# Performance work log

Measured on AMD Instinct MI355X. Metric: run time of the kernel, lower is better.

Reference implementation:

```python
import jax, jax.numpy as jnp
import numpy as np

HEAD_SIZE = 64
N_EMB = 384
B, S = 512, 256

def setup_inputs() -> dict:
    key = jax.random.key(0)
    k1, k2, k3, k4 = jax.random.split(key, 4)
    x = jax.random.normal(k1, (B, S, N_EMB), dtype=jnp.float32)
    scale = 1.0 / np.sqrt(N_EMB)
    Wq = jax.random.normal(k2, (N_EMB, HEAD_SIZE), dtype=jnp.float32) * scale
    Wk = jax.random.normal(k3, (N_EMB, HEAD_SIZE), dtype=jnp.float32) * scale
    Wv = jax.random.normal(k4, (N_EMB, HEAD_SIZE), dtype=jnp.float32) * scale
    return {"x": x, "Wq": Wq, "Wk": Wk, "Wv": Wv}

def reference(x, Wq, Wk, Wv):
    # Projections (Linear, no bias): [B,S,E] @ [E,H] -> [B,S,H]
    q = jnp.einsum('bse,eh->bsh', x, Wq)
    k = jnp.einsum('bse,eh->bsh', x, Wk)
    v = jnp.einsum('bse,eh->bsh', x, Wv)
    # Scores: [B,S,S], scaled by 1/sqrt(head_size)
    scores = jnp.einsum('bqh,bkh->bqk', q, k) / jnp.sqrt(jnp.asarray(HEAD_SIZE, x.dtype))
    seq_len = x.shape[1]
    causal = jnp.tril(jnp.ones((seq_len, seq_len), dtype=bool))
    scores = jnp.where(causal[None, :, :], scores, jnp.asarray(-jnp.inf, scores.dtype))
    attn = jax.nn.softmax(scores, axis=-1)
    # dropout_ratio=0 -> identity
    out = jnp.einsum('bqk,bkh->bqh', attn, v)
    return out
```

## Files before the change

kernel.cpp:

```cpp
#include <hip/hip_runtime.h>
#include <hip/hip_bf16.h>


#define NB   512
#define SS   256
#define EE   384
#define HH   64

#define PR16  16
#define LROW  392
#define XLSZ  (PR16 * LROW)

typedef short bf16x8 __attribute__((ext_vector_type(8)));
typedef float f32x4  __attribute__((ext_vector_type(4)));

__device__ __forceinline__ short f2bf(float f) {
  union { float f; unsigned u; } x; x.f = f;
  unsigned r = x.u + 0x7fffu + ((x.u >> 16) & 1u);
  return (short)(r >> 16);
}

__global__ __launch_bounds__(256) void prep_w_kernel(
    const float* __restrict__ Wq, const float* __restrict__ Wk,
    const float* __restrict__ Wv, short* __restrict__ wfrag) {
  int t = blockIdx.x * 256 + threadIdx.x;
  if (t >= 12 * 12 * 64) return;
  int ks  = t / (12 * 64);
  int rem = t % (12 * 64);
  int nf  = rem / 64;
  int l   = rem % 64;
  int l15 = l & 15, lhi = l >> 4;
  int ncat = nf * 16 + l15;
  const float* W = (ncat < 64) ? Wq : (ncat < 128 ? Wk : Wv);
  int n = ncat & 63;
  short* dst = wfrag + (size_t)t * 8;
#pragma unroll
  for (int j = 0; j < 8; ++j) {
    int kk = ks * 32 + lhi * 8 + j;
    dst[j] = f2bf(W[kk * 64 + n]);
  }
}

__global__ __launch_bounds__(512, 2) void fused_kernel(
    const float* __restrict__ x, const short* __restrict__ wfrag,
    float* __restrict__ out) {
  __shared__ short Ql[SS * HH];
  __shared__ short Kl[SS * HH];
  __shared__ short Vt[HH * SS];
  __shared__ short scratch[4 * XLSZ];

  int b    = blockIdx.x;
  int tid  = threadIdx.x;
  int lane = tid & 63, wv = tid >> 6;
  int l15  = lane & 15, lhi = lane >> 4;
  int g    = wv >> 2;
  int wg   = wv & 3;
  int tg   = tid & 255;
  const float* xg = x + (size_t)b * SS * EE + (size_t)g * 128 * EE;

  bf16x8 af[12][3];
#pragma unroll
  for (int ks = 0; ks < 12; ++ks)
#pragma unroll
    for (int h = 0; h < 3; ++h)
      af[ks][h] = *(const bf16x8*)(wfrag + ((size_t)(ks * 12 + wg * 3 + h) * 64 + lane) * 8);

  f32x4 st[6];

  auto loadch = [&](int ch) {
    const float* p0 = xg + (size_t)ch * (PR16 * EE);
#pragma unroll
    for (int i = 0; i < 3; ++i) {
      const f32x4* p = (const f32x4*)(p0 + (size_t)(tg + 256 * i) * 8);
      st[2 * i]     = p[0];
      st[2 * i + 1] = p[1];
    }
  };
  auto writech = [&](short* xl) {
#pragma unroll
    for (int i = 0; i < 3; ++i) {
      int c = tg + 256 * i;
      int row = c / 48, cg = c % 48;
      union { bf16x8 vv; __hip_bfloat162 h2[4]; } u;
      u.h2[0] = __float22bfloat162_rn(make_float2(st[2*i][0],   st[2*i][1]));
      u.h2[1] = __float22bfloat162_rn(make_float2(st[2*i][2],   st[2*i][3]));
      u.h2[2] = __float22bfloat162_rn(make_float2(st[2*i+1][0], st[2*i+1][1]));
      u.h2[3] = __float22bfloat162_rn(make_float2(st[2*i+1][2], st[2*i+1][3]));
      *(bf16x8*)(xl + row * LROW + cg * 8) = u.vv;
    }
  };

  loadch(0);
  writech(scratch + (g * 2) * XLSZ);

  for (int ch = 0; ch < 8; ++ch) {
    __syncthreads();
    if (ch < 7) loadch(ch + 1);
    const short* xl = scratch + (g * 2 + (ch & 1)) * XLSZ;

    f32x4 acc[3];
#pragma unroll
    for (int h = 0; h < 3; ++h) acc[h] = (f32x4){0.f, 0.f, 0.f, 0.f};

#pragma unroll
    for (int ks = 0; ks < 12; ++ks) {
      bf16x8 bx = *(const bf16x8*)(xl + l15 * LROW + ks * 32 + lhi * 8);
#pragma unroll
      for (int h = 0; h < 3; ++h)
        acc[h] = __builtin_amdgcn_mfma_f32_16x16x32_bf16(af[ks][h], bx, acc[h], 0, 0, 0);
    }

    int ncb = wg * 48 + lhi * 4;
    int row = g * 128 + ch * PR16 + l15;
#pragma unroll
    for (int ht = 0; ht < 3; ++ht) {
      int ncat = ncb + ht * 16;
      if (ncat < 128) {
        short* dst = (ncat < 64) ? Ql : Kl;
        int col = ncat & 63;
        union { short4 s4; __hip_bfloat162 h2[2]; } o;
        o.h2[0] = __float22bfloat162_rn(make_float2(acc[ht][0], acc[ht][1]));
        o.h2[1] = __float22bfloat162_rn(make_float2(acc[ht][2], acc[ht][3]));
        *(short4*)(dst + row * 64 + (col ^ ((row & 7) << 3))) = o.s4;
      } else {
#pragma unroll
        for (int j = 0; j < 4; ++j) {
          int h = ncat - 128 + j;
          Vt[h * 256 + (row ^ ((h & 7) << 3))] = f2bf(acc[ht][j]);
        }
      }
    }
    if (ch < 7) writech(scratch + (g * 2 + ((ch + 1) & 1)) * XLSZ);
  }
  __syncthreads();

  bf16x8 qa[2][2];
#pragma unroll
  for (int u = 0; u < 2; ++u) {
    int rt  = (u == 0) ? wv : (15 - wv);
    int row = rt * 16 + l15;
#pragma unroll
    for (int kf = 0; kf < 2; ++kf)
      qa[u][kf] = *(const bf16x8*)(Ql + row * 64 + ((kf * 32 + lhi * 8) ^ ((row & 7) << 3)));
  }
  __syncthreads();

  short* P = (wv < 6) ? (scratch + wv * (16 * 256)) : (Ql + (wv - 6) * (16 * 256));
  size_t obase = (size_t)b * SS * HH;

#pragma unroll
  for (int u = 0; u < 2; ++u) {
    int rt    = (u == 0) ? wv : (15 - wv);
    int qrow0 = rt * 16;
    int twp   = (rt + 2) & ~1;

    f32x4 s[16];
#pragma unroll
    for (int t = 0; t < 16; ++t) {
      if (t >= twp) continue;
      int kc = t * 16 + l15;
      bf16x8 kb0 = *(const bf16x8*)(Kl + kc * 64 + ((lhi * 8)      ^ ((kc & 7) << 3)));
      bf16x8 kb1 = *(const bf16x8*)(Kl + kc * 64 + ((32 + lhi * 8) ^ ((kc & 7) << 3)));
      f32x4 a = (f32x4){0.f, 0.f, 0.f, 0.f};
      a = __builtin_amdgcn_mfma_f32_16x16x32_bf16(qa[u][0], kb0, a, 0, 0, 0);
      a = __builtin_amdgcn_mfma_f32_16x16x32_bf16(qa[u][1], kb1, a, 0, 0, 0);
      s[t] = a;
    }

#pragma unroll
    for (int t = 0; t < 16; ++t) {
      if (t >= twp) continue;
      int col = t * 16 + l15;
#pragma unroll
      for (int r = 0; r < 4; ++r) {
        int qg = qrow0 + lhi * 4 + r;
        float val = s[t][r] * 0.125f;
        s[t][r] = (col > qg) ? -INFINITY : val;
      }
    }
    float mx[4], sm[4], inv[4];
#pragma unroll
    for (int r = 0; r < 4; ++r) mx[r] = -INFINITY;
#pragma unroll
    for (int t = 0; t < 16; ++t) {
      if (t >= twp) continue;
#pragma unroll
      for (int r = 0; r < 4; ++r) mx[r] = fmaxf(mx[r], s[t][r]);
    }
#pragma unroll
    for (int r = 0; r < 4; ++r) {
      mx[r] = fmaxf(mx[r], __shfl_xor(mx[r], 1));
      mx[r] = fmaxf(mx[r], __shfl_xor(mx[r], 2));
      mx[r] = fmaxf(mx[r], __shfl_xor(mx[r], 4));
      mx[r] = fmaxf(mx[r], __shfl_xor(mx[r], 8));
      sm[r] = 0.f;
    }
#pragma unroll
    for (int t = 0; t < 16; ++t) {
      if (t >= twp) continue;
#pragma unroll
      for (int r = 0; r < 4; ++r) {
        float p = __expf(s[t][r] - mx[r]);
        s[t][r] = p;
        sm[r] += p;
      }
    }
#pragma unroll
    for (int r = 0; r < 4; ++r) {
      sm[r] += __shfl_xor(sm[r], 1);
      sm[r] += __shfl_xor(sm[r], 2);
      sm[r] += __shfl_xor(sm[r], 4);
      sm[r] += __shfl_xor(sm[r], 8);
      inv[r] = 1.f / sm[r];
    }

#pragma unroll
    for (int t = 0; t < 16; ++t) {
      if (t >= twp) continue;
#pragma unroll
      for (int r = 0; r < 4; ++r) {
        int row = lhi * 4 + r;
        int col = t * 16 + l15;
        P[row * 256 + (col ^ ((row & 7) << 3))] = f2bf(s[t][r]);
      }
    }

    f32x4 o[4];
#pragma unroll
    for (int nf = 0; nf < 4; ++nf) o[nf] = (f32x4){0.f, 0.f, 0.f, 0.f};
    int nk = twp >> 1;
#pragma unroll
    for (int kc2 = 0; kc2 < 8; ++kc2) {
      if (kc2 >= nk) continue;
      int kofs = kc2 * 32 + lhi * 8;
      bf16x8 pa = *(const bf16x8*)(P + l15 * 256 + (kofs ^ ((l15 & 7) << 3)));
#pragma unroll
      for (int nf = 0; nf < 4; ++nf) {
        int hrow = nf * 16 + l15;
        bf16x8 vb = *(const bf16x8*)(Vt + hrow * 256 + (kofs ^ ((hrow & 7) << 3)));
        o[nf] = __builtin_amdgcn_mfma_f32_16x16x32_bf16(pa, vb, o[nf], 0, 0, 0);
      }
    }

#pragma unroll
    for (int nf = 0; nf < 4; ++nf)
#pragma unroll
      for (int r = 0; r < 4; ++r) {
        int qg = qrow0 + lhi * 4 + r;
        int h  = nf * 16 + l15;
        out[obase + (size_t)qg * HH + h] = o[nf][r] * inv[r];
      }
  }
}

extern "C" void kernel_launch(void* const* d_in, const int* in_sizes, int n_in,
                              void* d_out, int out_size, void* d_ws, size_t ws_size,
                              hipStream_t stream) {
  const float* x  = (const float*)d_in[0];
  const float* Wq = (const float*)d_in[1];
  const float* Wk = (const float*)d_in[2];
  const float* Wv = (const float*)d_in[3];
  float* out = (float*)d_out;

  short* wfrag = (short*)d_ws;

  prep_w_kernel<<<36, 256, 0, stream>>>(Wq, Wk, Wv, wfrag);
  fused_kernel<<<512, 512, 0, stream>>>(x, wfrag, out);
}
```

Before: 61.91 us.

## Restructure attention into 4-wave blocks with transposed scores and in-register P

Halves the block to 256 threads (4 waves), each computing 48 projection columns over 16 sequential row chunks, with a swizzled single x staging buffer. Q is no longer kept as a full tile in LDS: it goes through a small double-buffered ring and is loaded into registers per row tile. Attention now computes transposed scores (K as the A operand) so each lane owns one query row. Scores are recomputed in a max pass and again in a fused exp/PV pass, and the P fragment is packed directly in registers instead of round-tripping through LDS. This cuts LDS use and the P stores but recomputes QK^T and adds per-chunk barriers and a serial projection loop.

```diff
diff --git a/kernel.cpp b/kernel.cpp
--- a/kernel.cpp
+++ b/kernel.cpp
@@ -6,10 +6,6 @@
 #define SS   256
 #define EE   384
 #define HH   64
-
-#define PR16  16
-#define LROW  392
-#define XLSZ  (PR16 * LROW)
 
 typedef short bf16x8 __attribute__((ext_vector_type(8)));
 typedef float f32x4  __attribute__((ext_vector_type(4)));
@@ -41,87 +37,102 @@
   }
 }
 
-__global__ __launch_bounds__(512, 2) void fused_kernel(
+__global__ __launch_bounds__(256, 2) void fused_kernel(
     const float* __restrict__ x, const short* __restrict__ wfrag,
     float* __restrict__ out) {
-  __shared__ short Ql[SS * HH];
-  __shared__ short Kl[SS * HH];
-  __shared__ short Vt[HH * SS];
-  __shared__ short scratch[4 * XLSZ];
+  __shared__ __align__(16) short Kl[SS * HH];
+  __shared__ __align__(16) short Vt[HH * SS];
+  __shared__ __align__(16) short xst[16 * EE];
+  __shared__ __align__(16) short ring[2 * 16 * 64];
 
   int b    = blockIdx.x;
   int tid  = threadIdx.x;
   int lane = tid & 63, wv = tid >> 6;
   int l15  = lane & 15, lhi = lane >> 4;
-  int g    = wv >> 2;
-  int wg   = wv & 3;
-  int tg   = tid & 255;
-  const float* xg = x + (size_t)b * SS * EE + (size_t)g * 128 * EE;
+  int sw   = l15 & 7;
+  const float* xb = x + (size_t)b * SS * EE;
 
   bf16x8 af[12][3];
 #pragma unroll
   for (int ks = 0; ks < 12; ++ks)
 #pragma unroll
     for (int h = 0; h < 3; ++h)
-      af[ks][h] = *(const bf16x8*)(wfrag + ((size_t)(ks * 12 + wg * 3 + h) * 64 + lane) * 8);
+      af[ks][h] = *(const bf16x8*)(wfrag + ((size_t)(ks * 12 + wv * 3 + h) * 64 + lane) * 8);
 
   f32x4 st[6];
-
   auto loadch = [&](int ch) {
-    const float* p0 = xg + (size_t)ch * (PR16 * EE);
+    const float* p0 = xb + (size_t)ch * 16 * EE;
 #pragma unroll
     for (int i = 0; i < 3; ++i) {
-      const f32x4* p = (const f32x4*)(p0 + (size_t)(tg + 256 * i) * 8);
+      const f32x4* p = (const f32x4*)(p0 + (size_t)(tid + 256 * i) * 8);
       st[2 * i]     = p[0];
       st[2 * i + 1] = p[1];
     }
   };
-  auto writech = [&](short* xl) {
+  auto writech = [&]() {
 #pragma unroll
     for (int i = 0; i < 3; ++i) {
-      int c = tg + 256 * i;
+      int c = tid + 256 * i;
       int row = c / 48, cg = c % 48;
       union { bf16x8 vv; __hip_bfloat162 h2[4]; } u;
       u.h2[0] = __float22bfloat162_rn(make_float2(st[2*i][0],   st[2*i][1]));
       u.h2[1] = __float22bfloat162_rn(make_float2(st[2*i][2],   st[2*i][3]));
       u.h2[2] = __float22bfloat162_rn(make_float2(st[2*i+1][0], st[2*i+1][1]));
       u.h2[3] = __float22bfloat162_rn(make_float2(st[2*i+1][2], st[2*i+1][3]));
-      *(bf16x8*)(xl + row * LROW + cg * 8) = u.vv;
+      *(bf16x8*)(xst + row * 384 + ((cg ^ (row & 7)) * 8)) = u.vv;
     }
   };
 
+  bf16x8 qa[4][2];
+
   loadch(0);
-  writech(scratch + (g * 2) * XLSZ);
-
-  for (int ch = 0; ch < 8; ++ch) {
+  writech();
+  for (int ch = 0; ch < 16; ++ch) {
     __syncthreads();
-    if (ch < 7) loadch(ch + 1);
-    const short* xl = scratch + (g * 2 + (ch & 1)) * XLSZ;
+
+    if (ch >= 1) {
+      int rtp = ch - 1;
+      const short* slot = ring + (rtp & 1) * 1024;
+#pragma unroll
+      for (int uu = 0; uu < 4; ++uu) {
+        int rtu = (uu == 0) ? wv : (uu == 1) ? (7 - wv) : (uu == 2) ? (8 + wv) : (15 - wv);
+        if (rtp == rtu) {
+#pragma unroll
+          for (int kf = 0; kf < 2; ++kf)
+            qa[uu][kf] = *(const bf16x8*)(slot + l15 * 64 + ((kf * 32 + lhi * 8) ^ (sw << 3)));
+        }
+      }
+    }
+
+    if (ch < 15) loadch(ch + 1);
 
     f32x4 acc[3];
 #pragma unroll
     for (int h = 0; h < 3; ++h) acc[h] = (f32x4){0.f, 0.f, 0.f, 0.f};
-
 #pragma unroll
     for (int ks = 0; ks < 12; ++ks) {
-      bf16x8 bx = *(const bf16x8*)(xl + l15 * LROW + ks * 32 + lhi * 8);
+      bf16x8 bx = *(const bf16x8*)(xst + l15 * 384 + (((ks * 4 + lhi) ^ sw) * 8));
 #pragma unroll
       for (int h = 0; h < 3; ++h)
         acc[h] = __builtin_amdgcn_mfma_f32_16x16x32_bf16(af[ks][h], bx, acc[h], 0, 0, 0);
     }
 
-    int ncb = wg * 48 + lhi * 4;
-    int row = g * 128 + ch * PR16 + l15;
+    int row  = ch * 16 + l15;
+    int srow = ((row & 8) >> 1) | (row & 3);
 #pragma unroll
     for (int ht = 0; ht < 3; ++ht) {
-      int ncat = ncb + ht * 16;
-      if (ncat < 128) {
-        short* dst = (ncat < 64) ? Ql : Kl;
-        int col = ncat & 63;
+      int f = wv * 3 + ht;
+      int ncat = f * 16 + lhi * 4;
+      if (f < 8) {
         union { short4 s4; __hip_bfloat162 h2[2]; } o;
         o.h2[0] = __float22bfloat162_rn(make_float2(acc[ht][0], acc[ht][1]));
         o.h2[1] = __float22bfloat162_rn(make_float2(acc[ht][2], acc[ht][3]));
-        *(short4*)(dst + row * 64 + (col ^ ((row & 7) << 3))) = o.s4;
+        if (f < 4) {
+          *(short4*)(ring + (ch & 1) * 1024 + l15 * 64 + (ncat ^ (sw << 3))) = o.s4;
+        } else {
+          int col = ncat - 64;
+          *(short4*)(Kl + row * 64 + (col ^ (srow << 3))) = o.s4;
+        }
       } else {
 #pragma unroll
         for (int j = 0; j < 4; ++j) {
@@ -130,125 +141,104 @@
         }
       }
     }
-    if (ch < 7) writech(scratch + (g * 2 + ((ch + 1) & 1)) * XLSZ);
+    __syncthreads();
+    if (ch < 15) writech();
   }
   __syncthreads();
-
-  bf16x8 qa[2][2];
-#pragma unroll
-  for (int u = 0; u < 2; ++u) {
-    int rt  = (u == 0) ? wv : (15 - wv);
-    int row = rt * 16 + l15;
-#pragma unroll
-    for (int kf = 0; kf < 2; ++kf)
-      qa[u][kf] = *(const bf16x8*)(Ql + row * 64 + ((kf * 32 + lhi * 8) ^ ((row & 7) << 3)));
-  }
-  __syncthreads();
-
-  short* P = (wv < 6) ? (scratch + wv * (16 * 256)) : (Ql + (wv - 6) * (16 * 256));
+  {
+    const short* slot = ring + 1024;
+#pragma unroll
+    for (int uu = 0; uu < 4; ++uu) {
+      int rtu = (uu == 0) ? wv : (uu == 1) ? (7 - wv) : (uu == 2) ? (8 + wv) : (15 - wv);
+      if (rtu == 15) {
+#pragma unroll
+        for (int kf = 0; kf < 2; ++kf)
+          qa[uu][kf] = *(const bf16x8*)(slot + l15 * 64 + ((kf * 32 + lhi * 8) ^ (sw << 3)));
+      }
+    }
+  }
+
   size_t obase = (size_t)b * SS * HH;
-
-#pragma unroll
-  for (int u = 0; u < 2; ++u) {
-    int rt    = (u == 0) ? wv : (15 - wv);
+#pragma unroll
+  for (int u = 0; u < 4; ++u) {
+    int rt = (u == 0) ? wv : (u == 1) ? (7 - wv) : (u == 2) ? (8 + wv) : (15 - wv);
     int qrow0 = rt * 16;
-    int twp   = (rt + 2) & ~1;
-
-    f32x4 s[16];
-#pragma unroll
-    for (int t = 0; t < 16; ++t) {
-      if (t >= twp) continue;
-      int kc = t * 16 + l15;
-      bf16x8 kb0 = *(const bf16x8*)(Kl + kc * 64 + ((lhi * 8)      ^ ((kc & 7) << 3)));
-      bf16x8 kb1 = *(const bf16x8*)(Kl + kc * 64 + ((32 + lhi * 8) ^ ((kc & 7) << 3)));
+    int twp = (rt + 2) & ~1;
+    int nk  = twp >> 1;
+    int qg  = qrow0 + l15;
+
+    float mx = -3.0e38f;
+    for (int t = 0; t < twp; ++t) {
+      int kc = (t >> 1) * 32 + ((l15 >> 2) << 3) + ((t & 1) << 2) + (l15 & 3);
+      const short* kp = Kl + kc * 64;
+      bf16x8 kb0 = *(const bf16x8*)(kp + ((lhi * 8) ^ (sw << 3)));
+      bf16x8 kb1 = *(const bf16x8*)(kp + ((32 + lhi * 8) ^ (sw << 3)));
       f32x4 a = (f32x4){0.f, 0.f, 0.f, 0.f};
-      a = __builtin_amdgcn_mfma_f32_16x16x32_bf16(qa[u][0], kb0, a, 0, 0, 0);
-      a = __builtin_amdgcn_mfma_f32_16x16x32_bf16(qa[u][1], kb1, a, 0, 0, 0);
-      s[t] = a;
-    }
-
-#pragma unroll
-    for (int t = 0; t < 16; ++t) {
-      if (t >= twp) continue;
-      int col = t * 16 + l15;
+      a = __builtin_amdgcn_mfma_f32_16x16x32_bf16(kb0, qa[u][0], a, 0, 0, 0);
+      a = __builtin_amdgcn_mfma_f32_16x16x32_bf16(kb1, qa[u][1], a, 0, 0, 0);
 #pragma unroll
       for (int r = 0; r < 4; ++r) {
-        int qg = qrow0 + lhi * 4 + r;
-        float val = s[t][r] * 0.125f;
-        s[t][r] = (col > qg) ? -INFINITY : val;
-      }
-    }
-    float mx[4], sm[4], inv[4];
-#pragma unroll
-    for (int r = 0; r < 4; ++r) mx[r] = -INFINITY;
-#pragma unroll
-    for (int t = 0; t < 16; ++t) {
-      if (t >= twp) continue;
-#pragma unroll
-      for (int r = 0; r < 4; ++r) mx[r] = fmaxf(mx[r], s[t][r]);
-    }
-#pragma unroll
-    for (int r = 0; r < 4; ++r) {
-      mx[r] = fmaxf(mx[r], __shfl_xor(mx[r], 1));
-      mx[r] = fmaxf(mx[r], __shfl_xor(mx[r], 2));
-      mx[r] = fmaxf(mx[r], __shfl_xor(mx[r], 4));
-      mx[r] = fmaxf(mx[r], __shfl_xor(mx[r], 8));
-      sm[r] = 0.f;
-    }
-#pragma unroll
-    for (int t = 0; t < 16; ++t) {
-      if (t >= twp) continue;
+        int kg = (t >> 1) * 32 + lhi * 8 + ((t & 1) << 2) + r;
+        float v = a[r] * 0.125f;
+        mx = (kg <= qg) ? fmaxf(mx, v) : mx;
+      }
+    }
+    mx = fmaxf(mx, __shfl_xor(mx, 16));
+    mx = fmaxf(mx, __shfl_xor(mx, 32));
+
+    float sm = 0.f;
+    f32x4 o[4];
+#pragma unroll
+    for (int nf = 0; nf < 4; ++nf) o[nf] = (f32x4){0.f, 0.f, 0.f, 0.f};
+    for (int kc2 = 0; kc2 < nk; ++kc2) {
+      int kcA = kc2 * 32 + ((l15 >> 2) << 3) + (l15 & 3);
+      const short* kpA = Kl + kcA * 64;
+      const short* kpB = kpA + 4 * 64;
+      bf16x8 a0 = *(const bf16x8*)(kpA + ((lhi * 8) ^ (sw << 3)));
+      bf16x8 a1 = *(const bf16x8*)(kpA + ((32 + lhi * 8) ^ (sw << 3)));
+      bf16x8 b0 = *(const bf16x8*)(kpB + ((lhi * 8) ^ (sw << 3)));
+      bf16x8 b1 = *(const bf16x8*)(kpB + ((32 + lhi * 8) ^ (sw << 3)));
+      f32x4 aA = (f32x4){0.f, 0.f, 0.f, 0.f};
+      aA = __builtin_amdgcn_mfma_f32_16x16x32_bf16(a0, qa[u][0], aA, 0, 0, 0);
+      aA = __builtin_amdgcn_mfma_f32_16x16x32_bf16(a1, qa[u][1], aA, 0, 0, 0);
+      f32x4 aB = (f32x4){0.f, 0.f, 0.f, 0.f};
+      aB = __builtin_amdgcn_mfma_f32_16x16x32_bf16(b0, qa[u][0], aB, 0, 0, 0);
+      aB = __builtin_amdgcn_mfma_f32_16x16x32_bf16(b1, qa[u][1], aB, 0, 0, 0);
+      float pA[4], pB[4];
 #pragma unroll
       for (int r = 0; r < 4; ++r) {
-        float p = __expf(s[t][r] - mx[r]);
-        s[t][r] = p;
-        sm[r] += p;
-      }
-    }
-#pragma unroll
-    for (int r = 0; r < 4; ++r) {
-      sm[r] += __shfl_xor(sm[r], 1);
-      sm[r] += __shfl_xor(sm[r], 2);
-      sm[r] += __shfl_xor(sm[r], 4);
-      sm[r] += __shfl_xor(sm[r], 8);
-      inv[r] = 1.f / sm[r];
-    }
-
-#pragma unroll
-    for (int t = 0; t < 16; ++t) {
-      if (t >= twp) continue;
-#pragma unroll
-      for (int r = 0; r < 4; ++r) {
-        int row = lhi * 4 + r;
-        int col = t * 16 + l15;
-        P[row * 256 + (col ^ ((row & 7) << 3))] = f2bf(s[t][r]);
-      }
-    }
-
-    f32x4 o[4];
-#pragma unroll
-    for (int nf = 0; nf < 4; ++nf) o[nf] = (f32x4){0.f, 0.f, 0.f, 0.f};
-    int nk = twp >> 1;
-#pragma unroll
-    for (int kc2 = 0; kc2 < 8; ++kc2) {
-      if (kc2 >= nk) continue;
+        int kgA = kc2 * 32 + lhi * 8 + r;
+        pA[r] = (kgA <= qg) ? __expf(aA[r] * 0.125f - mx) : 0.f;
+        pB[r] = (kgA + 4 <= qg) ? __expf(aB[r] * 0.125f - mx) : 0.f;
+        sm += pA[r] + pB[r];
+      }
+      union { bf16x8 v; __hip_bfloat162 h2[4]; } pu;
+      pu.h2[0] = __float22bfloat162_rn(make_float2(pA[0], pA[1]));
+      pu.h2[1] = __float22bfloat162_rn(make_float2(pA[2], pA[3]));
+      pu.h2[2] = __float22bfloat162_rn(make_float2(pB[0], pB[1]));
+      pu.h2[3] = __float22bfloat162_rn(make_float2(pB[2], pB[3]));
       int kofs = kc2 * 32 + lhi * 8;
-      bf16x8 pa = *(const bf16x8*)(P + l15 * 256 + (kofs ^ ((l15 & 7) << 3)));
 #pragma unroll
       for (int nf = 0; nf < 4; ++nf) {
         int hrow = nf * 16 + l15;
         bf16x8 vb = *(const bf16x8*)(Vt + hrow * 256 + (kofs ^ ((hrow & 7) << 3)));
-        o[nf] = __builtin_amdgcn_mfma_f32_16x16x32_bf16(pa, vb, o[nf], 0, 0, 0);
-      }
-    }
+        o[nf] = __builtin_amdgcn_mfma_f32_16x16x32_bf16(pu.v, vb, o[nf], 0, 0, 0);
+      }
+    }
+    sm += __shfl_xor(sm, 16);
+    sm += __shfl_xor(sm, 32);
+    float inv = 1.f / sm;
+    float invq[4];
+#pragma unroll
+    for (int r = 0; r < 4; ++r) invq[r] = __shfl(inv, lhi * 4 + r);
 
 #pragma unroll
     for (int nf = 0; nf < 4; ++nf)
 #pragma unroll
       for (int r = 0; r < 4; ++r) {
-        int qg = qrow0 + lhi * 4 + r;
-        int h  = nf * 16 + l15;
-        out[obase + (size_t)qg * HH + h] = o[nf][r] * inv[r];
+        int q = qrow0 + lhi * 4 + r;
+        int h = nf * 16 + l15;
+        out[obase + (size_t)q * HH + h] = o[nf][r] * invq[r];
       }
   }
 }
@@ -265,5 +255,5 @@
   short* wfrag = (short*)d_ws;
 
   prep_w_kernel<<<36, 256, 0, stream>>>(Wq, Wk, Wv, wfrag);
-  fused_kernel<<<512, 512, 0, stream>>>(x, wfrag, out);
-}
+  fused_kernel<<<512, 256, 0, stream>>>(x, wfrag, out);
+}
```

After: 67.07 us. 8.3% more time.
